# Performance work log

Measured on AMD Instinct MI355X. Metric: run time of the kernel, lower is better.

The kernel has to match this reference:

```python
import math
import jax, jax.numpy as jnp
import numpy as np

ALPHA = 0.2  # LeakyReLU negative slope
MASK_VAL = -9e15


def _positional_encoding(n: int, d: int) -> jnp.ndarray:
    # Custom PE with a (1 + exp(-pos/100)) decay factor, matching CustomPositionalEncoding
    position = jnp.arange(n, dtype=jnp.float32)[:, None]            # [N,1]
    div_term = jnp.exp(jnp.arange(0, d, 2, dtype=jnp.float32) * (-math.log(10000.0) / d))
    decay = 1.0 + jnp.exp(-position / 100.0)                         # [N,1]
    pe = jnp.zeros((n, d), dtype=jnp.float32)
    pe = pe.at[:, 0::2].set(jnp.sin(position * div_term) * decay)
    pe = pe.at[:, 1::2].set(jnp.cos(position * div_term) * decay)
    return pe[None]                                                  # [1,N,d]


def setup_inputs() -> dict:
    key = jax.random.key(0)
    k_h, k_adj, k_W, k_a = jax.random.split(key, 4)
    B, N, IN_F, OUT_F = 8, 2048, 128, 128
    h = jax.random.normal(k_h, (B, N, IN_F), dtype=jnp.float32)
    # sparse-ish 0/1 adjacency (float, as in the torch module)
    adj = jax.random.randint(k_adj, (B, N, N), 0, 2).astype(jnp.float32)
    # xavier_uniform init scale
    limW = math.sqrt(6.0 / (IN_F + OUT_F))
    W = jax.random.uniform(k_W, (IN_F, OUT_F), minval=-limW, maxval=limW, dtype=jnp.float32)
    lima = math.sqrt(6.0 / (2 * OUT_F + 1))
    a = jax.random.uniform(k_a, (2 * OUT_F, 1), minval=-lima, maxval=lima, dtype=jnp.float32)
    return {"h": h, "adj": adj, "W": W, "a": a}


def reference(h, adj, W, a):
    B, N, _ = h.shape
    out_f = W.shape[1]
    h = h + _positional_encoding(N, h.shape[2])
    # force self-loops
    eye = jnp.eye(N, dtype=adj.dtype)[None]
    adj = jnp.where(eye > 0, jnp.ones_like(adj), adj)
    Wh = jnp.einsum('bni,io->bno', h, W)                 # [B,N,out_f]
    a1 = a[:out_f, 0]
    a2 = a[out_f:, 0]
    s1 = Wh @ a1                                          # [B,N]
    s2 = Wh @ a2                                          # [B,N]
    e = s1[:, :, None] + s2[:, None, :]                   # [B,N,N] additive score
    e = jnp.where(e >= 0, e, ALPHA * e)                   # leaky relu
    attn = jnp.where(adj > 0, e, MASK_VAL)
    attn = jax.nn.softmax(attn, axis=-1)
    # dropout is identity in eval mode
    h_prime = jnp.einsum('bnm,bmo->bno', attn, Wh)        # [B,N,out_f]
    deg = adj.sum(-1)                                     # [B,N]
    valid = deg > 0
    valid = valid.at[:, 0].set(False)
    denom = jnp.clip(valid.sum(1, keepdims=True), 1, None).astype(h_prime.dtype)  # [B,1]
    g = (h_prime * valid[:, :, None]).sum(1) / denom      # [B,out_f] masked mean pool
    return jax.nn.elu(g)
```

## Files before the change

kernel.cpp:

```cpp
#include <hip/hip_runtime.h>
#include <math.h>

#define NN 2048
#define BATCH 8
#define FDIM 128
#define MASKV -9000000000000000.0f

__global__ void k_pe(float* __restrict__ pe) {
    int i = blockIdx.x * 256 + threadIdx.x;
    int n = i >> 7;
    int k = i & 127;
    int jj = k >> 1;
    float dt = expf((float)(2 * jj) * (-0.07195578415606394f));
    float ang = (float)n * dt;
    float decay = 1.f + expf(-(float)n * 0.01f);
    float v = ((k & 1) == 0 ? sinf(ang) : cosf(ang)) * decay;
    pe[i] = v;
}

__global__ __launch_bounds__(256) void k_wh(const float* __restrict__ h,
                                            const float* __restrict__ pe,
                                            const float* __restrict__ W,
                                            const float* __restrict__ a,
                                            float* __restrict__ Wh,
                                            float* __restrict__ s1,
                                            float* __restrict__ s2) {
    __shared__ float w_lds[64 * 128];
    __shared__ float hpe_lds[64 * 68];
    const int b  = blockIdx.y;
    const int n0 = blockIdx.x * 64;
    const int t  = threadIdx.x;
    const int tc = t & 15;
    const int tr = t >> 4;

    float acc[4][8];
#pragma unroll
    for (int i = 0; i < 4; i++)
#pragma unroll
        for (int j = 0; j < 8; j++) acc[i][j] = 0.f;

    for (int kp = 0; kp < 2; ++kp) {
        {
            const float4* wsrc = (const float4*)(W + kp * 64 * 128);
            float4* wdst = (float4*)w_lds;
#pragma unroll
            for (int q = 0; q < 8; q++) wdst[t + q * 256] = wsrc[t + q * 256];
        }
        {
#pragma unroll
            for (int q = 0; q < 4; q++) {
                int f = t + q * 256;
                int r = f >> 4;
                int k4 = (f & 15) << 2;
                int n = n0 + r;
                int kk = kp * 64 + k4;
                const float* hp_src = h + ((size_t)b * NN + n) * FDIM + kk;
                float4 hv = *(const float4*)hp_src;
                float4 pv = *(const float4*)(pe + (size_t)n * FDIM + kk);
                float4 hpv = make_float4(hv.x + pv.x, hv.y + pv.y,
                                         hv.z + pv.z, hv.w + pv.w);
                *(float4*)(hpe_lds + r * 68 + k4) = hpv;
            }
        }
        __syncthreads();
#pragma unroll 4
        for (int k = 0; k < 64; k++) {
            float wv[8];
            float4 wa = *(float4*)(w_lds + k * 128 + tc * 8);
            float4 wb = *(float4*)(w_lds + k * 128 + tc * 8 + 4);
            wv[0] = wa.x; wv[1] = wa.y; wv[2] = wa.z; wv[3] = wa.w;
            wv[4] = wb.x; wv[5] = wb.y; wv[6] = wb.z; wv[7] = wb.w;
#pragma unroll
            for (int i = 0; i < 4; i++) {
                float hv = hpe_lds[(tr * 4 + i) * 68 + k];
#pragma unroll
                for (int j = 0; j < 8; j++) acc[i][j] = fmaf(hv, wv[j], acc[i][j]);
            }
        }
        __syncthreads();
    }

    float a1v[8], a2v[8];
#pragma unroll
    for (int j = 0; j < 8; j++) { a1v[j] = a[tc * 8 + j]; a2v[j] = a[FDIM + tc * 8 + j]; }
#pragma unroll
    for (int i = 0; i < 4; i++) {
        int n = n0 + tr * 4 + i;
        float* dst = Wh + ((size_t)b * NN + n) * FDIM + tc * 8;
        *(float4*)dst = make_float4(acc[i][0], acc[i][1], acc[i][2], acc[i][3]);
        *(float4*)(dst + 4) = make_float4(acc[i][4], acc[i][5], acc[i][6], acc[i][7]);
        float p1 = 0.f, p2 = 0.f;
#pragma unroll
        for (int j = 0; j < 8; j++) {
            p1 = fmaf(acc[i][j], a1v[j], p1);
            p2 = fmaf(acc[i][j], a2v[j], p2);
        }
#pragma unroll
        for (int off = 1; off < 16; off <<= 1) {
            p1 += __shfl_xor(p1, off, 64);
            p2 += __shfl_xor(p2, off, 64);
        }
        if (tc == 0) {
            s1[(size_t)b * NN + n] = p1;
            s2[(size_t)b * NN + n] = p2;
        }
    }
}

__global__ __launch_bounds__(256) void k_attn(const float* __restrict__ adj,
                                              const float* __restrict__ s1,
                                              const float* __restrict__ s2,
                                              float* __restrict__ c_part) {
    const int b = blockIdx.y;
    const int chunk = blockIdx.x;
    const int t = threadIdx.x;
    const int wave = t >> 6;
    const int lane = t & 63;
    __shared__ float c_lds[4][NN];

    const float* s2b = s2 + (size_t)b * NN;
    float s2v[32];
#pragma unroll
    for (int kq = 0; kq < 8; kq++) {
        float4 v = *(const float4*)(s2b + kq * 256 + lane * 4);
        s2v[kq * 4 + 0] = v.x; s2v[kq * 4 + 1] = v.y;
        s2v[kq * 4 + 2] = v.z; s2v[kq * 4 + 3] = v.w;
    }
    float c_acc[32];
#pragma unroll
    for (int j = 0; j < 32; j++) c_acc[j] = 0.f;

    const int nbase = chunk * 16;
    const float* adjb = adj + (size_t)b * NN * NN;
    const float* s1b = s1 + (size_t)b * NN;

#pragma unroll 1
    for (int ri = 0; ri < 4; ri++) {
        int n = nbase + wave * 4 + ri;
        if (n == 0) continue;
        float s1n = s1b[n];
        const float* arow = adjb + (size_t)n * NN;
        float val[32];
        float vmax = MASKV;
#pragma unroll
        for (int kq = 0; kq < 8; kq++) {
            float4 av = *(const float4*)(arow + kq * 256 + lane * 4);
            float a4[4] = {av.x, av.y, av.z, av.w};
#pragma unroll
            for (int e = 0; e < 4; e++) {
                int m = kq * 256 + lane * 4 + e;
                float x = s1n + s2v[kq * 4 + e];
                float ev = fmaxf(x, 0.2f * x);
                bool conn = (a4[e] > 0.f) || (m == n);
                float v = conn ? ev : MASKV;
                val[kq * 4 + e] = v;
                vmax = fmaxf(vmax, v);
            }
        }
#pragma unroll
        for (int off = 32; off; off >>= 1) vmax = fmaxf(vmax, __shfl_xor(vmax, off, 64));
        float zsum = 0.f;
#pragma unroll
        for (int j = 0; j < 32; j++) {
            float p = __expf(val[j] - vmax);
            val[j] = p;
            zsum += p;
        }
#pragma unroll
        for (int off = 32; off; off >>= 1) zsum += __shfl_xor(zsum, off, 64);
        float rz = 1.f / zsum;
#pragma unroll
        for (int j = 0; j < 32; j++) c_acc[j] = fmaf(val[j], rz, c_acc[j]);
    }

#pragma unroll
    for (int kq = 0; kq < 8; kq++)
        *(float4*)(&c_lds[wave][kq * 256 + lane * 4]) =
            make_float4(c_acc[kq * 4 + 0], c_acc[kq * 4 + 1],
                        c_acc[kq * 4 + 2], c_acc[kq * 4 + 3]);
    __syncthreads();
    float* dst = c_part + ((size_t)b * 128 + chunk) * NN;
#pragma unroll
    for (int q = 0; q < 2; q++) {
        int idx = t + q * 256;
        float4 v0 = ((float4*)c_lds[0])[idx];
        float4 v1 = ((float4*)c_lds[1])[idx];
        float4 v2 = ((float4*)c_lds[2])[idx];
        float4 v3 = ((float4*)c_lds[3])[idx];
        ((float4*)dst)[idx] = make_float4(v0.x + v1.x + v2.x + v3.x,
                                          v0.y + v1.y + v2.y + v3.y,
                                          v0.z + v1.z + v2.z + v3.z,
                                          v0.w + v1.w + v2.w + v3.w);
    }
}

__global__ __launch_bounds__(256) void k_gpre(const float* __restrict__ Wh,
                                              const float* __restrict__ c_part,
                                              float* __restrict__ g_part) {
    const int b = blockIdx.y;
    const int mc = blockIdx.x;
    const int m0 = mc * 64;
    const int t = threadIdx.x;
    __shared__ float red[256];
    __shared__ float c_lds[64];

    {
        const int mi = t & 63;
        const int w = t >> 6;
        const float* cp = c_part + (size_t)b * 128 * NN + m0 + mi;
        float s = 0.f;
#pragma unroll 8
        for (int j = 0; j < 32; j++) s += cp[(size_t)(w * 32 + j) * NN];
        red[w * 64 + mi] = s;
    }
    __syncthreads();
    if (t < 64) c_lds[t] = red[t] + red[t + 64] + red[t + 128] + red[t + 192];
    __syncthreads();

    const int o = t & 127;
    const int mh = t >> 7;
    float acc = 0.f;
    const float* whb = Wh + ((size_t)b * NN + m0 + mh * 32) * FDIM;
#pragma unroll 4
    for (int mm = 0; mm < 32; mm++)
        acc = fmaf(c_lds[mh * 32 + mm], whb[mm * FDIM + o], acc);
    g_part[((size_t)(mc * 2 + mh)) * (BATCH * FDIM) + b * FDIM + o] = acc;
}

__global__ void k_elu(const float* __restrict__ g_part, float* __restrict__ out) {
    int i = blockIdx.x * 256 + threadIdx.x;
    if (i < BATCH * FDIM) {
        float s = 0.f;
#pragma unroll 8
        for (int p = 0; p < 64; p++) s += g_part[p * (BATCH * FDIM) + i];
        float g = s * (1.0f / 2047.0f);
        out[i] = g > 0.f ? g : expm1f(g);
    }
}

extern "C" void kernel_launch(void* const* d_in, const int* in_sizes, int n_in,
                              void* d_out, int out_size, void* d_ws, size_t ws_size,
                              hipStream_t stream) {
    (void)in_sizes; (void)n_in; (void)out_size; (void)ws_size;
    const float* h   = (const float*)d_in[0];
    const float* adj = (const float*)d_in[1];
    const float* W   = (const float*)d_in[2];
    const float* a   = (const float*)d_in[3];
    float* out = (float*)d_out;

    char* ws = (char*)d_ws;
    float* Wh     = (float*)ws;
    float* pe     = Wh + (size_t)BATCH * NN * FDIM;
    float* s1     = pe + (size_t)NN * FDIM;
    float* s2     = s1 + (size_t)BATCH * NN;
    float* c_part = s2 + (size_t)BATCH * NN;
    float* g_part = c_part + (size_t)BATCH * 128 * NN;

    hipLaunchKernelGGL(k_pe, dim3(NN * FDIM / 256), dim3(256), 0, stream, pe);
    hipLaunchKernelGGL(k_wh, dim3(NN / 64, BATCH), dim3(256), 0, stream,
                       h, pe, W, a, Wh, s1, s2);
    hipLaunchKernelGGL(k_attn, dim3(NN / 16, BATCH), dim3(256), 0, stream,
                       adj, s1, s2, c_part);
    hipLaunchKernelGGL(k_gpre, dim3(NN / 64, BATCH), dim3(256), 0, stream,
                       Wh, c_part, g_part);
    hipLaunchKernelGGL(k_elu, dim3(4), dim3(256), 0, stream, g_part, out);
}
```

Measured before the change: 226.9 us.

## Drop softmax max pass, use bitmask recompute, shrink LDS, widen k_wh blocks

The attention kernel no longer keeps 32 masked scores per row or computes a row max. It stores a 32-bit connectivity mask, accumulates exp(score) directly, and recomputes the exponentials after normalisation. This frees registers and removes the max reduction, and it assumes the scores are small enough that exp does not overflow. The per-wave LDS partials are replaced with one LDS array filled by shared atomics, which cuts LDS use and may raise occupancy. k_wh now uses 512 threads per block with two rows per thread.

```diff
diff --git a/kernel.cpp b/kernel.cpp
--- a/kernel.cpp
+++ b/kernel.cpp
@@ -4,7 +4,6 @@
 #define NN 2048
 #define BATCH 8
 #define FDIM 128
-#define MASKV -9000000000000000.0f
 
 __global__ void k_pe(float* __restrict__ pe) {
     int i = blockIdx.x * 256 + threadIdx.x;
@@ -18,7 +17,7 @@
     pe[i] = v;
 }
 
-__global__ __launch_bounds__(256) void k_wh(const float* __restrict__ h,
+__global__ __launch_bounds__(512) void k_wh(const float* __restrict__ h,
                                             const float* __restrict__ pe,
                                             const float* __restrict__ W,
                                             const float* __restrict__ a,
@@ -33,9 +32,9 @@
     const int tc = t & 15;
     const int tr = t >> 4;
 
-    float acc[4][8];
-#pragma unroll
-    for (int i = 0; i < 4; i++)
+    float acc[2][8];
+#pragma unroll
+    for (int i = 0; i < 2; i++)
 #pragma unroll
         for (int j = 0; j < 8; j++) acc[i][j] = 0.f;
 
@@ -44,22 +43,20 @@
             const float4* wsrc = (const float4*)(W + kp * 64 * 128);
             float4* wdst = (float4*)w_lds;
 #pragma unroll
-            for (int q = 0; q < 8; q++) wdst[t + q * 256] = wsrc[t + q * 256];
+            for (int q = 0; q < 4; q++) wdst[t + q * 512] = wsrc[t + q * 512];
         }
         {
 #pragma unroll
-            for (int q = 0; q < 4; q++) {
-                int f = t + q * 256;
+            for (int q = 0; q < 2; q++) {
+                int f = t + q * 512;
                 int r = f >> 4;
                 int k4 = (f & 15) << 2;
                 int n = n0 + r;
                 int kk = kp * 64 + k4;
-                const float* hp_src = h + ((size_t)b * NN + n) * FDIM + kk;
-                float4 hv = *(const float4*)hp_src;
+                float4 hv = *(const float4*)(h + ((size_t)b * NN + n) * FDIM + kk);
                 float4 pv = *(const float4*)(pe + (size_t)n * FDIM + kk);
-                float4 hpv = make_float4(hv.x + pv.x, hv.y + pv.y,
-                                         hv.z + pv.z, hv.w + pv.w);
-                *(float4*)(hpe_lds + r * 68 + k4) = hpv;
+                *(float4*)(hpe_lds + r * 68 + k4) =
+                    make_float4(hv.x + pv.x, hv.y + pv.y, hv.z + pv.z, hv.w + pv.w);
             }
         }
         __syncthreads();
@@ -71,8 +68,8 @@
             wv[0] = wa.x; wv[1] = wa.y; wv[2] = wa.z; wv[3] = wa.w;
             wv[4] = wb.x; wv[5] = wb.y; wv[6] = wb.z; wv[7] = wb.w;
 #pragma unroll
-            for (int i = 0; i < 4; i++) {
-                float hv = hpe_lds[(tr * 4 + i) * 68 + k];
+            for (int i = 0; i < 2; i++) {
+                float hv = hpe_lds[(tr * 2 + i) * 68 + k];
 #pragma unroll
                 for (int j = 0; j < 8; j++) acc[i][j] = fmaf(hv, wv[j], acc[i][j]);
             }
@@ -84,8 +81,8 @@
 #pragma unroll
     for (int j = 0; j < 8; j++) { a1v[j] = a[tc * 8 + j]; a2v[j] = a[FDIM + tc * 8 + j]; }
 #pragma unroll
-    for (int i = 0; i < 4; i++) {
-        int n = n0 + tr * 4 + i;
+    for (int i = 0; i < 2; i++) {
+        int n = n0 + tr * 2 + i;
         float* dst = Wh + ((size_t)b * NN + n) * FDIM + tc * 8;
         *(float4*)dst = make_float4(acc[i][0], acc[i][1], acc[i][2], acc[i][3]);
         *(float4*)(dst + 4) = make_float4(acc[i][4], acc[i][5], acc[i][6], acc[i][7]);
@@ -116,7 +113,9 @@
     const int t = threadIdx.x;
     const int wave = t >> 6;
     const int lane = t & 63;
-    __shared__ float c_lds[4][NN];
+    __shared__ float c_lds[NN];
+    for (int i = t; i < NN; i += 256) c_lds[i] = 0.f;
+    __syncthreads();
 
     const float* s2b = s2 + (size_t)b * NN;
     float s2v[32];
@@ -140,57 +139,50 @@
         if (n == 0) continue;
         float s1n = s1b[n];
         const float* arow = adjb + (size_t)n * NN;
-        float val[32];
-        float vmax = MASKV;
+        unsigned mask = 0u;
+        float zsum = 0.f;
 #pragma unroll
         for (int kq = 0; kq < 8; kq++) {
             float4 av = *(const float4*)(arow + kq * 256 + lane * 4);
             float a4[4] = {av.x, av.y, av.z, av.w};
 #pragma unroll
             for (int e = 0; e < 4; e++) {
+                int j = kq * 4 + e;
                 int m = kq * 256 + lane * 4 + e;
-                float x = s1n + s2v[kq * 4 + e];
+                float x = s1n + s2v[j];
                 float ev = fmaxf(x, 0.2f * x);
                 bool conn = (a4[e] > 0.f) || (m == n);
-                float v = conn ? ev : MASKV;
-                val[kq * 4 + e] = v;
-                vmax = fmaxf(vmax, v);
-            }
-        }
-#pragma unroll
-        for (int off = 32; off; off >>= 1) vmax = fmaxf(vmax, __shfl_xor(vmax, off, 64));
-        float zsum = 0.f;
-#pragma unroll
-        for (int j = 0; j < 32; j++) {
-            float p = __expf(val[j] - vmax);
-            val[j] = p;
-            zsum += p;
+                mask |= (unsigned)conn << j;
+                zsum += conn ? __expf(ev) : 0.f;
+            }
         }
 #pragma unroll
         for (int off = 32; off; off >>= 1) zsum += __shfl_xor(zsum, off, 64);
         float rz = 1.f / zsum;
 #pragma unroll
-        for (int j = 0; j < 32; j++) c_acc[j] = fmaf(val[j], rz, c_acc[j]);
+        for (int kq = 0; kq < 8; kq++)
+#pragma unroll
+            for (int e = 0; e < 4; e++) {
+                int j = kq * 4 + e;
+                float x = s1n + s2v[j];
+                float ev = fmaxf(x, 0.2f * x);
+                float p = ((mask >> j) & 1u) ? __expf(ev) : 0.f;
+                c_acc[j] = fmaf(p, rz, c_acc[j]);
+            }
     }
 
 #pragma unroll
     for (int kq = 0; kq < 8; kq++)
-        *(float4*)(&c_lds[wave][kq * 256 + lane * 4]) =
-            make_float4(c_acc[kq * 4 + 0], c_acc[kq * 4 + 1],
-                        c_acc[kq * 4 + 2], c_acc[kq * 4 + 3]);
-    __syncthreads();
+#pragma unroll
+        for (int e = 0; e < 4; e++)
+            atomicAdd(&c_lds[kq * 256 + lane * 4 + e], c_acc[kq * 4 + e]);
+    __syncthreads();
+
     float* dst = c_part + ((size_t)b * 128 + chunk) * NN;
 #pragma unroll
     for (int q = 0; q < 2; q++) {
         int idx = t + q * 256;
-        float4 v0 = ((float4*)c_lds[0])[idx];
-        float4 v1 = ((float4*)c_lds[1])[idx];
-        float4 v2 = ((float4*)c_lds[2])[idx];
-        float4 v3 = ((float4*)c_lds[3])[idx];
-        ((float4*)dst)[idx] = make_float4(v0.x + v1.x + v2.x + v3.x,
-                                          v0.y + v1.y + v2.y + v3.y,
-                                          v0.z + v1.z + v2.z + v3.z,
-                                          v0.w + v1.w + v2.w + v3.w);
+        ((float4*)dst)[idx] = ((const float4*)c_lds)[idx];
     }
 }
 
@@ -257,7 +249,7 @@
     float* g_part = c_part + (size_t)BATCH * 128 * NN;
 
     hipLaunchKernelGGL(k_pe, dim3(NN * FDIM / 256), dim3(256), 0, stream, pe);
-    hipLaunchKernelGGL(k_wh, dim3(NN / 64, BATCH), dim3(256), 0, stream,
+    hipLaunchKernelGGL(k_wh, dim3(NN / 64, BATCH), dim3(512), 0, stream,
                        h, pe, W, a, Wh, s1, s2);
     hipLaunchKernelGGL(k_attn, dim3(NN / 16, BATCH), dim3(256), 0, stream,
                        adj, s1, s2, c_part);
```

Result: slower. 259.6 us (+14.4%).
